# Optimization experiments

Measured on AMD Instinct MI355X. Metric: run time of the kernel, lower is better.

Reference implementation:

```python
import jax, jax.numpy as jnp
import numpy as np

T = 2048      # time steps (X.shape[0])
D = 64        # input_dim (= future_dim)
H = 1024      # hidden_dim
OUT = 64      # output_dim
ND = 3        # num_decoders


def setup_inputs() -> dict:
    key = jax.random.key(0)
    ks = jax.random.split(key, 20)
    def p(k, shape, scale=0.03):
        return jax.random.normal(k, shape, dtype=jnp.float32) * scale
    return {
        "X": jax.random.normal(ks[0], (T, D), dtype=jnp.float32),
        # enc LSTMCell: input = fusion_dim = 2*D
        "enc_Wih": p(ks[1], (4 * H, 2 * D)), "enc_Whh": p(ks[2], (4 * H, H)),
        "enc_bih": p(ks[3], (4 * H,)), "enc_bhh": p(ks[4], (4 * H,)),
        # dec LSTMCell: input = H
        "dec_Wih": p(ks[5], (4 * H, H)), "dec_Whh": p(ks[6], (4 * H, H)),
        "dec_bih": p(ks[7], (4 * H,)), "dec_bhh": p(ks[8], (4 * H,)),
        # fc_relu heads
        "hx_W": p(ks[9], (H, H)), "hx_b": p(ks[10], (H,)),
        "cx_W": p(ks[11], (H, H)), "cx_b": p(ks[12], (H,)),
        "fus_W": p(ks[13], (H, OUT)), "fus_b": p(ks[14], (H,)),
        "fut_W": p(ks[15], (D, H)), "fut_b": p(ks[16], (D,)),
        # classifier (shared by encoder and decoder)
        "cls_W": p(ks[17], (OUT, H)), "cls_b": p(ks[18], (OUT,)),
    }


def _lstm_cell(x, h, c, Wih, Whh, bih, bhh):
    # torch.nn.LSTMCell gate order: i, f, g, o
    g = x @ Wih.T + bih + h @ Whh.T + bhh
    i, f, gg, o = jnp.split(g, 4, axis=-1)
    c_new = jax.nn.sigmoid(f) * c + jax.nn.sigmoid(i) * jnp.tanh(gg)
    h_new = jax.nn.sigmoid(o) * jnp.tanh(c_new)
    return h_new, c_new


def reference(X, enc_Wih, enc_Whh, enc_bih, enc_bhh,
              dec_Wih, dec_Whh, dec_bih, dec_bhh,
              hx_W, hx_b, cx_W, cx_b, fus_W, fus_b,
              fut_W, fut_b, cls_W, cls_b):
    relu = jax.nn.relu

    def step(carry, x_t):
        enc_hx, enc_cx, fut = carry  # [H], [H], [D]
        fusion = jnp.concatenate([x_t, fut])  # [2D]
        enc_hx, enc_cx = _lstm_cell(fusion, enc_hx, enc_cx,
                                    enc_Wih, enc_Whh, enc_bih, enc_bhh)
        enc_score = enc_hx @ cls_W.T + cls_b  # [OUT]
        dhx = relu(enc_hx @ hx_W.T + hx_b)
        dcx = relu(enc_cx @ cx_W.T + cx_b)
        fusion_in = jnp.zeros((H,), X.dtype)
        fut_new = jnp.zeros((D,), X.dtype)
        dscores = []
        for _ in range(ND):
            # Original bug preserved: decoder returns the UNCHANGED cx
            # (`decc_cx` typo), so dcx is never updated inside this loop.
            dhx, _unused_cx = _lstm_cell(fusion_in, dhx, dcx,
                                         dec_Wih, dec_Whh, dec_bih, dec_bhh)
            ds = dhx @ cls_W.T + cls_b
            dscores.append(ds)
            fusion_in = relu(ds @ fus_W.T + fus_b)
            fut_new = fut_new + relu(dhx @ fut_W.T + fut_b)
        fut_new = fut_new / ND
        return (enc_hx, enc_cx, fut_new), (enc_score, jnp.stack(dscores))

    init = (jnp.zeros((H,), X.dtype), jnp.zeros((H,), X.dtype),
            jnp.zeros((D,), X.dtype))
    _, (enc_scores, dec_scores) = jax.lax.scan(step, init, X[: T - ND])
    # enc_scores: [T-ND, OUT]; dec_scores: [T-ND, ND, OUT] -> [(T-ND)*ND, OUT]
    return enc_scores, dec_scores.reshape(-1, OUT)
```

## Files before the change

kernel.cpp:

```cpp
#include <hip/hip_runtime.h>
#include <hip/hip_bf16.h>


typedef unsigned short u16t;
typedef unsigned int u32t;
typedef unsigned long long u64t;

#define TSTEPS 2045
#define NWG 256
#define NTHR 512
#define SPINCAP 8192

#define HENC  0
#define CENC  4096
#define DHX   8192
#define DD1   12288
#define DD2   16384
#define DD3   20480
#define SFF   24576

struct Params {
  const void *X, *eWih, *eWhh, *ebih, *ebhh, *dWih, *dWhh, *dbih, *dbhh,
             *hxW, *hxb, *cxW, *cxb, *fusW, *fusb_g, *futW, *futb_g, *clsW, *clsb_g;
  float* ws;
  void* out;
};

struct SharedMem {
  alignas(16) float encW[16 * 1152];
  alignas(16) u16t  decW[16 * 2048];
  alignas(16) float xs[2048];
  alignas(16) float xsf[128];
  float clsb[64], futb[64], fut_acc[64], dsbuf[64], fv3[64], xnext[64];
  float bias_e[16], bias_d[16], g16[16];
  float dcx_s[4], encc[4], hxb4[4], cxb4[4];
  int bail;
  int badcnt;
};

__device__ __forceinline__ float bfu(u16t u){
  union { u32t i; float f; } v; v.i = ((u32t)u) << 16; return v.f;
}
__device__ __forceinline__ u32t fbits(float f){
  union { float f; u32t u; } c; c.f = f; return c.u;
}
__device__ __forceinline__ u16t bf16bits(float v){
  __hip_bfloat16 b = __float2bfloat16(v);
  union { __hip_bfloat16 b; u16t u; } c; c.b = b; return c.u;
}
template<bool F32>
__device__ __forceinline__ float ldE(const void* p, int i){
  if (F32) return ((const float*)p)[i];
  return bfu(((const u16t*)p)[i]);
}
template<bool F32>
__device__ __forceinline__ u16t ldB(const void* p, int i){
  if (F32) return bf16bits(((const float*)p)[i]);
  return ((const u16t*)p)[i];
}
template<bool F32>
__device__ __forceinline__ void stO(void* p, int i, float v){
  if (F32) ((float*)p)[i] = v;
  else     ((u16t*)p)[i] = bf16bits(v);
}
__device__ __forceinline__ float sigm(float x){ return 1.f / (1.f + __expf(-x)); }
__device__ __forceinline__ float tanhx(float x){
  float e = __expf(-2.f * fabsf(x));
  float t = (1.f - e) / (1.f + e);
  return copysignf(t, x);
}
__device__ __forceinline__ void backoff(int sp){
  if (sp > 8)      __builtin_amdgcn_s_sleep(8);
  else if (sp > 2) __builtin_amdgcn_s_sleep(2);
}
__device__ __forceinline__ void stp(float* rowbase, int idx, float v, u32t ep){
  u64t u = (u64t)fbits(v) | ((u64t)ep << 32);
  __hip_atomic_store((u64t*)rowbase + idx, u,
                     __ATOMIC_RELAXED, __HIP_MEMORY_SCOPE_AGENT);
}
__device__ __forceinline__ float4 ld4c(const float* p){
  float4 r;
  asm volatile("global_load_dwordx4 %0, %1, off sc0 sc1\n\t"
               "s_waitcnt vmcnt(0)"
               : "=&v"(r) : "v"(p) : "memory");
  return r;
}
__device__ __forceinline__ void ld4c2(const float* p0, const float* p1,
                                      float4& a, float4& b){
  asm volatile(
    "global_load_dwordx4 %0, %2, off sc0 sc1\n\t"
    "global_load_dwordx4 %1, %3, off sc0 sc1\n\t"
    "s_waitcnt vmcnt(0)"
    : "=&v"(a), "=&v"(b)
    : "v"(p0), "v"(p1)
    : "memory");
}
__device__ __forceinline__ float2 poll2(const float* q, u32t ep, int* bail){
  float4 r; int sp = 0;
  for (;;){
    r = ld4c(q);
    if (fbits(r.y) == ep && fbits(r.w) == ep) break;
    if (*bail) break;
    if (++sp > SPINCAP){ *bail = 1; break; }
    backoff(sp);
  }
  return float2{r.x, r.z};
}

template<bool F32>
__device__ __forceinline__ float hw_dot(const void* wbase, long off,
                                        const float* __restrict__ x,
                                        int K, int lane){
  float acc = 0.f;
  if (F32){
    const float* w = (const float*)wbase + off;
    for (int c = lane * 4; c < K; c += 128){
      float4 wv = *(const float4*)(w + c);
      float4 xv = *(const float4*)(x + c);
      acc = fmaf(wv.x, xv.x, acc); acc = fmaf(wv.y, xv.y, acc);
      acc = fmaf(wv.z, xv.z, acc); acc = fmaf(wv.w, xv.w, acc);
    }
  } else {
    const u16t* w = (const u16t*)wbase + off;
    for (int c = lane * 4; c < K; c += 128){
      ushort4 wv = *(const ushort4*)(w + c);
      float4  xv = *(const float4*)(x + c);
      acc = fmaf(bfu(wv.x), xv.x, acc); acc = fmaf(bfu(wv.y), xv.y, acc);
      acc = fmaf(bfu(wv.z), xv.z, acc); acc = fmaf(bfu(wv.w), xv.w, acc);
    }
  }
  #pragma unroll
  for (int o = 16; o; o >>= 1) acc += __shfl_xor(acc, o, 64);
  return acc;
}

__device__ __forceinline__ float dotnr_f32(const float* __restrict__ w,
                                           const float* __restrict__ x,
                                           int K, int lane){
  float acc = 0.f;
  for (int c = lane * 4; c < K; c += 128){
    float4 wv = *(const float4*)(w + c);
    float4 xv = *(const float4*)(x + c);
    acc = fmaf(wv.x, xv.x, acc); acc = fmaf(wv.y, xv.y, acc);
    acc = fmaf(wv.z, xv.z, acc); acc = fmaf(wv.w, xv.w, acc);
  }
  return acc;
}
__device__ __forceinline__ float wred(float a){
  #pragma unroll
  for (int o = 16; o; o >>= 1) a += __shfl_xor(a, o, 64);
  return a;
}

__device__ __forceinline__ float lds_dot_bf16(const u16t* __restrict__ w,
                                              const float* __restrict__ x,
                                              int K, int lane){
  float acc = 0.f;
  for (int c = lane * 8; c < K; c += 256){
    uint4  wv = *(const uint4*)(w + c);
    float4 x0 = *(const float4*)(x + c);
    float4 x1 = *(const float4*)(x + c + 4);
    acc = fmaf(bfu((u16t)(wv.x & 0xffff)), x0.x, acc);
    acc = fmaf(bfu((u16t)(wv.x >> 16)),    x0.y, acc);
    acc = fmaf(bfu((u16t)(wv.y & 0xffff)), x0.z, acc);
    acc = fmaf(bfu((u16t)(wv.y >> 16)),    x0.w, acc);
    acc = fmaf(bfu((u16t)(wv.z & 0xffff)), x1.x, acc);
    acc = fmaf(bfu((u16t)(wv.z >> 16)),    x1.y, acc);
    acc = fmaf(bfu((u16t)(wv.w & 0xffff)), x1.z, acc);
    acc = fmaf(bfu((u16t)(wv.w >> 16)),    x1.w, acc);
  }
  #pragma unroll
  for (int o = 16; o; o >>= 1) acc += __shfl_xor(acc, o, 64);
  return acc;
}

template<bool F32>
__device__ __forceinline__ void produce_sf(const Params& p, float* ws,
                                           SharedMem& S, int ph, int par,
                                           u32t ep, int t, int w, int hw,
                                           int lane){
  const int o = (w & 7) * 16 + hw;
  float* sf = ws + SFF + (par * 3 + ph) * 256;
  if (o < 64){
    float s = hw_dot<F32>(p.clsW, (long)o * 1024, S.xs + 1024, 1024, lane)
            + S.clsb[o];
    if (lane == 0){
      stO<F32>(p.out, TSTEPS * 64 + (t * 3 + ph) * 64 + o, s);
      if (ph < 2) stp(sf, o, s, ep);
    }
  } else {
    float s = fmaxf(hw_dot<F32>(p.futW, (long)(o - 64) * 1024, S.xs + 1024, 1024, lane)
                    + S.futb[o - 64], 0.f);
    if (lane == 0) stp(sf, o, s, ep);
  }
}

template<bool F32>
__device__ void run(const Params& p, SharedMem& S){
  const int tid  = threadIdx.x;
  const int w    = blockIdx.x;
  const int hw   = tid >> 5;
  const int lane = tid & 31;
  const long grow = (long)((hw >> 2) * 1024 + 4 * w + (hw & 3));
  float* ws = p.ws;

  {
    float* er = S.encW + hw * 1152;
    for (int c = lane; c < 128; c += 32)  er[c]       = ldE<F32>(p.eWih, (int)(grow * 128 + c));
    for (int c = lane; c < 1024; c += 32) er[128 + c] = ldE<F32>(p.eWhh, (int)(grow * 1024 + c));
    u16t* dr = S.decW + hw * 2048;
    for (int c = lane; c < 1024; c += 32){
      dr[c]        = ldB<F32>(p.dWih, (int)(grow * 1024 + c));
      dr[1024 + c] = ldB<F32>(p.dWhh, (int)(grow * 1024 + c));
    }
  }
  u32t fw[64];
  float fusb0, fusb1;
  {
    int h0 = 2 * tid, h1 = 2 * tid + 1;
    #pragma unroll
    for (int o = 0; o < 64; ++o){
      u16t lo = ldB<F32>(p.fusW, h0 * 64 + o);
      u16t hi = ldB<F32>(p.fusW, h1 * 64 + o);
      fw[o] = ((u32t)hi << 16) | lo;
    }
    fusb0 = ldE<F32>(p.fusb_g, h0);
    fusb1 = ldE<F32>(p.fusb_g, h1);
  }
  if (tid < 64){
    S.clsb[tid] = ldE<F32>(p.clsb_g, tid);
    S.futb[tid] = ldE<F32>(p.futb_g, tid);
    S.fut_acc[tid] = 0.f;
  }
  if (tid < 16){
    int gr = (tid >> 2) * 1024 + 4 * w + (tid & 3);
    S.bias_e[tid] = ldE<F32>(p.ebih, gr) + ldE<F32>(p.ebhh, gr);
    S.bias_d[tid] = ldE<F32>(p.dbih, gr) + ldE<F32>(p.dbhh, gr);
  }
  if (tid < 4){
    S.hxb4[tid] = ldE<F32>(p.hxb, 4 * w + tid);
    S.cxb4[tid] = ldE<F32>(p.cxb, 4 * w + tid);
    S.encc[tid] = 0.f;
  }
  float enc_pre = 0.f;
  __syncthreads();

  for (int t = 0; t < TSTEPS; ++t){
    const int  par  = t & 1;
    const int  ppar = par ^ 1;
    const u32t ep   = (u32t)(t + 1);
    const u32t epv  = (u32t)t;

    if (t > 0 && tid < 32){
      const float* base = ws + SFF + (ppar * 3 + 2) * 256;
      float2 v = poll2(base + (32 + tid) * 4, epv, &S.bail);
      S.fv3[2 * tid] = v.x; S.fv3[2 * tid + 1] = v.y;
    }
    __syncthreads();
    if (tid < 64){
      S.xsf[tid] = (t == 0) ? ldE<F32>(p.X, tid) : S.xnext[tid];
      float fv = (t > 0) ? (S.fut_acc[tid] + S.fv3[tid]) * (1.f / 3.f) : 0.f;
      S.xsf[64 + tid] = fv;
      S.fut_acc[tid] = 0.f;
    }
    __syncthreads();
    {
      float a = wred(enc_pre + dotnr_f32(S.encW + hw * 1152, S.xsf, 128, lane))
              + S.bias_e[hw];
      if (lane == 0) S.g16[hw] = a;
    }
    __syncthreads();
    if (tid < 4){
      float gi = sigm(S.g16[tid]), gf = sigm(S.g16[4 + tid]),
            gg = tanhx(S.g16[8 + tid]), go = sigm(S.g16[12 + tid]);
      float c = gf * S.encc[tid] + gi * gg;
      float h = go * tanhx(c);
      S.encc[tid] = c;
      stp(ws + HENC + par * 2048, 4 * w + tid, h, ep);
      stp(ws + CENC + par * 2048, 4 * w + tid, c, ep);
    }

    {
      const float* ph_ = ws + HENC + par * 2048 + tid * 4;
      const float* pc_ = ws + CENC + par * 2048 + tid * 4;
      float4 a, b; int sp = 0;
      for (;;){
        ld4c2(ph_, pc_, a, b);
        if (fbits(a.y) == ep && fbits(a.w) == ep &&
            fbits(b.y) == ep && fbits(b.w) == ep) break;
        if (S.bail) break;
        if (++sp > SPINCAP){ S.bail = 1; break; }
        backoff(sp);
      }
      S.xs[2 * tid] = a.x;        S.xs[2 * tid + 1] = a.z;
      S.xs[1024 + 2 * tid] = b.x; S.xs[1025 + 2 * tid] = b.z;
    }
    __syncthreads();
    if (hw < 4){
      float d = fmaxf(hw_dot<F32>(p.hxW, (long)(4 * w + hw) * 1024, S.xs, 1024, lane)
                      + S.hxb4[hw], 0.f);
      if (lane == 0) stp(ws + DHX + par * 2048, 4 * w + hw, d, ep);
    } else if (hw < 8){
      int j = hw - 4;
      float d = fmaxf(hw_dot<F32>(p.cxW, (long)(4 * w + j) * 1024, S.xs + 1024, 1024, lane)
                      + S.cxb4[j], 0.f);
      if (lane == 0) S.dcx_s[j] = d;
    } else if (w >= 8 && w < 16){
      int r = (w - 8) * 8 + (hw - 8);
      float s = hw_dot<F32>(p.clsW, (long)r * 1024, S.xs, 1024, lane) + S.clsb[r];
      if (lane == 0) stO<F32>(p.out, t * 64 + r, s);
    }
    enc_pre = dotnr_f32(S.encW + hw * 1152 + 128, S.xs, 1024, lane);
    __syncthreads();

    {
      float2 v = poll2(ws + DHX + par * 2048 + tid * 4, ep, &S.bail);
      S.xs[2 * tid] = v.x; S.xs[2 * tid + 1] = v.y;
    }
    __syncthreads();
    {
      float a = lds_dot_bf16(S.decW + hw * 2048 + 1024, S.xs, 1024, lane) + S.bias_d[hw];
      if (lane == 0) S.g16[hw] = a;
    }
    __syncthreads();
    if (tid < 4){
      float gi = sigm(S.g16[tid]), gf = sigm(S.g16[4 + tid]),
            gg = tanhx(S.g16[8 + tid]), go = sigm(S.g16[12 + tid]);
      float c = gf * S.dcx_s[tid] + gi * gg;
      float h = go * tanhx(c);
      stp(ws + DD1 + par * 2048, 4 * w + tid, h, ep);
    }
    if (tid < 64)
      S.xnext[tid] = ldE<F32>(p.X, (t + 1) * 64 + tid);

    for (int di = 2; di <= 3; ++di){
      const int ph = di - 2;
      {
        const float* dbuf = ws + (di == 2 ? DD1 : DD2) + par * 2048;
        float2 v = poll2(dbuf + tid * 4, ep, &S.bail);
        S.xs[1024 + 2 * tid] = v.x; S.xs[1025 + 2 * tid] = v.y;
      }
      __syncthreads();
      if (w >= 16 + ph * 8 && w < 24 + ph * 8)
        produce_sf<F32>(p, ws, S, ph, par, ep, t, w, hw, lane);
      float accA = lds_dot_bf16(S.decW + hw * 2048 + 1024, S.xs + 1024, 1024, lane);
      if (tid < 64){
        const float* sf = ws + SFF + (par * 3 + ph) * 256;
        float2 v = poll2(sf + tid * 4, ep, &S.bail);
        if (tid < 32){ S.dsbuf[2 * tid] = v.x; S.dsbuf[2 * tid + 1] = v.y; }
        else { S.fv3[2 * (tid - 32)] = v.x; S.fv3[2 * (tid - 32) + 1] = v.y; }
      }
      __syncthreads();
      if (tid < 64) S.fut_acc[tid] += S.fv3[tid];
      {
        float a0 = fusb0, a1 = fusb1;
        #pragma unroll
        for (int o = 0; o < 64; ++o){
          float d = S.dsbuf[o];
          a0 = fmaf(bfu((u16t)(fw[o] & 0xffff)), d, a0);
          a1 = fmaf(bfu((u16t)(fw[o] >> 16)),    d, a1);
        }
        S.xs[2 * tid]     = fmaxf(a0, 0.f);
        S.xs[2 * tid + 1] = fmaxf(a1, 0.f);
      }
      __syncthreads();
      float accB = lds_dot_bf16(S.decW + hw * 2048, S.xs, 1024, lane);
      {
        float a = accA + accB + S.bias_d[hw];
        if (lane == 0) S.g16[hw] = a;
      }
      __syncthreads();
      if (tid < 4){
        float gi = sigm(S.g16[tid]), gf = sigm(S.g16[4 + tid]),
              gg = tanhx(S.g16[8 + tid]), go = sigm(S.g16[12 + tid]);
        float c = gf * S.dcx_s[tid] + gi * gg;
        float h = go * tanhx(c);
        stp(ws + (di == 2 ? DD2 : DD3) + par * 2048, 4 * w + tid, h, ep);
      }
    }
    if (w >= 32 && w < 40){
      {
        float2 v = poll2(ws + DD3 + par * 2048 + tid * 4, ep, &S.bail);
        S.xs[1024 + 2 * tid] = v.x; S.xs[1025 + 2 * tid] = v.y;
      }
      __syncthreads();
      produce_sf<F32>(p, ws, S, 2, par, ep, t, w, hw, lane);
    }
  }
}

__global__ __launch_bounds__(NTHR, 2)
void trn_persist(Params p){
  __shared__ SharedMem S;
  if (threadIdx.x == 0){ S.bail = 0; S.badcnt = 0; }
  __syncthreads();
  if (threadIdx.x < 256){
    u16t u = ((const u16t*)p.X)[threadIdx.x];
    int e = (u >> 7) & 0xff;
    if (e == 0 || e >= 141) atomicAdd(&S.badcnt, 1);
  }
  __syncthreads();
  if (S.badcnt >= 3) run<true>(p, S);
  else               run<false>(p, S);
}

extern "C" void kernel_launch(void* const* d_in, const int* in_sizes, int n_in,
                              void* d_out, int out_size, void* d_ws, size_t ws_size,
                              hipStream_t stream){
  Params P;
  P.X      = d_in[0];
  P.eWih   = d_in[1];
  P.eWhh   = d_in[2];
  P.ebih   = d_in[3];
  P.ebhh   = d_in[4];
  P.dWih   = d_in[5];
  P.dWhh   = d_in[6];
  P.dbih   = d_in[7];
  P.dbhh   = d_in[8];
  P.hxW    = d_in[9];
  P.hxb    = d_in[10];
  P.cxW    = d_in[11];
  P.cxb    = d_in[12];
  P.fusW   = d_in[13];
  P.fusb_g = d_in[14];
  P.futW   = d_in[15];
  P.futb_g = d_in[16];
  P.clsW   = d_in[17];
  P.clsb_g = d_in[18];
  P.ws     = (float*)d_ws;
  P.out    = d_out;

  void* args[] = { &P };
  hipLaunchCooperativeKernel((void*)trn_persist, dim3(NWG), dim3(NTHR),
                             args, 0, stream);
}
```

Measured before the change: 51.04 ms.

## Cache hx/cx head weights in LDS and pre-convert cls/fut rows to bf16

Moves the per-workgroup hx_W and cx_W rows into shared memory as bf16 so they are no longer streamed from global memory every step. It also stores the encoder Whh slice as bf16 to make room in LDS. The cls/fut rows used by the score producers are converted once into a bf16 scratch area in the workspace. The aim is to cut per-timestep global weight traffic on the serial critical path, at the cost of extra bf16 rounding of encoder recurrent weights and larger LDS use, which may reduce occupancy.

```diff
diff --git a/kernel.cpp b/kernel.cpp
--- a/kernel.cpp
+++ b/kernel.cpp
@@ -18,6 +18,7 @@
 #define DD2   16384
 #define DD3   20480
 #define SFF   24576
+#define BCW   28672
 
 struct Params {
   const void *X, *eWih, *eWhh, *ebih, *ebhh, *dWih, *dWhh, *dbih, *dbhh,
@@ -27,8 +28,10 @@
 };
 
 struct SharedMem {
-  alignas(16) float encW[16 * 1152];
+  alignas(16) float encWih[16 * 128];
+  alignas(16) u16t  encWhh[16 * 1024];
   alignas(16) u16t  decW[16 * 2048];
+  alignas(16) u16t  headW[8 * 1024];
   alignas(16) float xs[2048];
   alignas(16) float xsf[128];
   float clsb[64], futb[64], fut_acc[64], dsbuf[64], fv3[64], xnext[64];
@@ -146,15 +149,9 @@
   }
   return acc;
 }
-__device__ __forceinline__ float wred(float a){
-  #pragma unroll
-  for (int o = 16; o; o >>= 1) a += __shfl_xor(a, o, 64);
-  return a;
-}
-
-__device__ __forceinline__ float lds_dot_bf16(const u16t* __restrict__ w,
-                                              const float* __restrict__ x,
-                                              int K, int lane){
+__device__ __forceinline__ float dotnr_bf16(const u16t* __restrict__ w,
+                                            const float* __restrict__ x,
+                                            int K, int lane){
   float acc = 0.f;
   for (int c = lane * 8; c < K; c += 256){
     uint4  wv = *(const uint4*)(w + c);
@@ -169,28 +166,36 @@
     acc = fmaf(bfu((u16t)(wv.w & 0xffff)), x1.z, acc);
     acc = fmaf(bfu((u16t)(wv.w >> 16)),    x1.w, acc);
   }
+  return acc;
+}
+__device__ __forceinline__ float wred(float a){
   #pragma unroll
-  for (int o = 16; o; o >>= 1) acc += __shfl_xor(acc, o, 64);
-  return acc;
+  for (int o = 16; o; o >>= 1) a += __shfl_xor(a, o, 64);
+  return a;
+}
+__device__ __forceinline__ float lds_dot_bf16(const u16t* __restrict__ w,
+                                              const float* __restrict__ x,
+                                              int K, int lane){
+  return wred(dotnr_bf16(w, x, K, lane));
 }
 
 template<bool F32>
 __device__ __forceinline__ void produce_sf(const Params& p, float* ws,
+                                           const u16t* __restrict__ myrow,
                                            SharedMem& S, int ph, int par,
                                            u32t ep, int t, int w, int hw,
                                            int lane){
   const int o = (w & 7) * 16 + hw;
   float* sf = ws + SFF + (par * 3 + ph) * 256;
+  float s = hw_dot<false>(myrow, 0, S.xs + 1024, 1024, lane);
   if (o < 64){
-    float s = hw_dot<F32>(p.clsW, (long)o * 1024, S.xs + 1024, 1024, lane)
-            + S.clsb[o];
+    s += S.clsb[o];
     if (lane == 0){
       stO<F32>(p.out, TSTEPS * 64 + (t * 3 + ph) * 64 + o, s);
       if (ph < 2) stp(sf, o, s, ep);
     }
   } else {
-    float s = fmaxf(hw_dot<F32>(p.futW, (long)(o - 64) * 1024, S.xs + 1024, 1024, lane)
-                    + S.futb[o - 64], 0.f);
+    s = fmaxf(s + S.futb[o - 64], 0.f);
     if (lane == 0) stp(sf, o, s, ep);
   }
 }
@@ -203,16 +208,34 @@
   const int lane = tid & 31;
   const long grow = (long)((hw >> 2) * 1024 + 4 * w + (hw & 3));
   float* ws = p.ws;
+  u16t* bcw = (u16t*)(ws + BCW);
 
   {
-    float* er = S.encW + hw * 1152;
-    for (int c = lane; c < 128; c += 32)  er[c]       = ldE<F32>(p.eWih, (int)(grow * 128 + c));
-    for (int c = lane; c < 1024; c += 32) er[128 + c] = ldE<F32>(p.eWhh, (int)(grow * 1024 + c));
+    float* ei = S.encWih + hw * 128;
+    for (int c = lane; c < 128; c += 32)  ei[c] = ldE<F32>(p.eWih, (int)(grow * 128 + c));
+    u16t* eh = S.encWhh + hw * 1024;
+    for (int c = lane; c < 1024; c += 32) eh[c] = ldB<F32>(p.eWhh, (int)(grow * 1024 + c));
     u16t* dr = S.decW + hw * 2048;
     for (int c = lane; c < 1024; c += 32){
       dr[c]        = ldB<F32>(p.dWih, (int)(grow * 1024 + c));
       dr[1024 + c] = ldB<F32>(p.dWhh, (int)(grow * 1024 + c));
     }
+  }
+  for (int i = tid; i < 8192; i += NTHR){
+    int r = i >> 10, c = i & 1023;
+    S.headW[i] = (r < 4) ? ldB<F32>(p.hxW, (4 * w + r) * 1024 + c)
+                         : ldB<F32>(p.cxW, (4 * w + (r - 4)) * 1024 + c);
+  }
+  const u16t* myrow = nullptr;
+  if (w >= 16 && w < 40){
+    const int slot = (w - 16) * 16 + hw;
+    const int o = (w & 7) * 16 + hw;
+    const void* src = (o < 64) ? p.clsW : p.futW;
+    const int row = (o < 64) ? o : o - 64;
+    u16t* dst = bcw + (size_t)slot * 1024;
+    for (int c = lane; c < 1024; c += 32)
+      dst[c] = ldB<F32>(src, row * 1024 + c);
+    myrow = dst;
   }
   u32t fw[64];
   float fusb0, fusb1;
@@ -265,7 +288,7 @@
     }
     __syncthreads();
     {
-      float a = wred(enc_pre + dotnr_f32(S.encW + hw * 1152, S.xsf, 128, lane))
+      float a = wred(enc_pre + dotnr_f32(S.encWih + hw * 128, S.xsf, 128, lane))
               + S.bias_e[hw];
       if (lane == 0) S.g16[hw] = a;
     }
@@ -297,12 +320,12 @@
     }
     __syncthreads();
     if (hw < 4){
-      float d = fmaxf(hw_dot<F32>(p.hxW, (long)(4 * w + hw) * 1024, S.xs, 1024, lane)
+      float d = fmaxf(lds_dot_bf16(S.headW + hw * 1024, S.xs, 1024, lane)
                       + S.hxb4[hw], 0.f);
       if (lane == 0) stp(ws + DHX + par * 2048, 4 * w + hw, d, ep);
     } else if (hw < 8){
       int j = hw - 4;
-      float d = fmaxf(hw_dot<F32>(p.cxW, (long)(4 * w + j) * 1024, S.xs + 1024, 1024, lane)
+      float d = fmaxf(lds_dot_bf16(S.headW + (4 + j) * 1024, S.xs + 1024, 1024, lane)
                       + S.cxb4[j], 0.f);
       if (lane == 0) S.dcx_s[j] = d;
     } else if (w >= 8 && w < 16){
@@ -310,7 +333,7 @@
       float s = hw_dot<F32>(p.clsW, (long)r * 1024, S.xs, 1024, lane) + S.clsb[r];
       if (lane == 0) stO<F32>(p.out, t * 64 + r, s);
     }
-    enc_pre = dotnr_f32(S.encW + hw * 1152 + 128, S.xs, 1024, lane);
+    enc_pre = dotnr_bf16(S.encWhh + hw * 1024, S.xs, 1024, lane);
     __syncthreads();
 
     {
@@ -342,7 +365,7 @@
       }
       __syncthreads();
       if (w >= 16 + ph * 8 && w < 24 + ph * 8)
-        produce_sf<F32>(p, ws, S, ph, par, ep, t, w, hw, lane);
+        produce_sf<F32>(p, ws, myrow, S, ph, par, ep, t, w, hw, lane);
       float accA = lds_dot_bf16(S.decW + hw * 2048 + 1024, S.xs + 1024, 1024, lane);
       if (tid < 64){
         const float* sf = ws + SFF + (par * 3 + ph) * 256;
@@ -384,7 +407,7 @@
         S.xs[1024 + 2 * tid] = v.x; S.xs[1025 + 2 * tid] = v.y;
       }
       __syncthreads();
-      produce_sf<F32>(p, ws, S, 2, par, ep, t, w, hw, lane);
+      produce_sf<F32>(p, ws, myrow, S, 2, par, ep, t, w, hw, lane);
     }
   }
 }
```

Result: faster. 49.54 ms (-2.9%).
